# Performance work log

Hardware: AMD Instinct MI355X
Metric: run time of the kernel (lower is better)

The kernel has to match this reference:

```python
import jax, jax.numpy as jnp
import numpy as np

B, S, D, H, E, K, F = 2, 2048, 1024, 16, 8, 2, 4096
DH = D // H
EPS = 1e-5


def setup_inputs() -> dict:
    key = jax.random.key(0)
    ks = jax.random.split(key, 10)
    init = lambda k, shape, scale: (jax.random.normal(k, shape, jnp.float32) * scale)
    s_d = D ** -0.5
    s_f = F ** -0.5
    return {
        "x": init(ks[0], (B, S, D), 1.0),
        "attn_mask": jnp.tril(jnp.ones((S, S), bool)),  # causal boolean mask
        "wq": init(ks[1], (D, D), s_d),
        "wk": init(ks[2], (D, D), s_d),
        "wv": init(ks[3], (D, D), s_d),
        "wo": init(ks[4], (D, D), s_d),
        "ln1_g": jnp.ones((D,), jnp.float32),
        "ln1_b": jnp.zeros((D,), jnp.float32),
        "ln2_g": jnp.ones((D,), jnp.float32),
        "ln2_b": jnp.zeros((D,), jnp.float32),
        "gate_w": init(ks[5], (D, E), s_d),
        "e_w1": init(ks[6], (E, D, F), s_d),
        "e_b1": jnp.zeros((E, F), jnp.float32),
        "e_w2": init(ks[7], (E, F, D), s_f),
        "e_b2": jnp.zeros((E, D), jnp.float32),
    }


def _ln(x, g, b):
    m = x.mean(-1, keepdims=True)
    v = ((x - m) ** 2).mean(-1, keepdims=True)
    return (x - m) * jax.lax.rsqrt(v + EPS) * g + b


def _mha(x, attn_mask, wq, wk, wv, wo):
    # x: [B,S,D] -> q,k,v: [B,H,S,DH]
    q = (x @ wq).reshape(B, S, H, DH).transpose(0, 2, 1, 3)
    k = (x @ wk).reshape(B, S, H, DH).transpose(0, 2, 1, 3)
    v = (x @ wv).reshape(B, S, H, DH).transpose(0, 2, 1, 3)
    scores = jnp.einsum("bhqd,bhkd->bhqk", q, k) * (DH ** -0.5)
    scores = jnp.where(attn_mask, scores, jnp.finfo(scores.dtype).min)
    attn = jax.nn.softmax(scores, axis=-1)
    o = jnp.einsum("bhqk,bhkd->bhqd", attn, v)
    return o.transpose(0, 2, 1, 3).reshape(B, S, D) @ wo


def _moe(x, gate_w, e_w1, e_b1, e_w2, e_b2):
    tokens = x.reshape(-1, D)  # [N,D]
    logits = tokens @ gate_w   # [N,E]
    vals, idx = jax.lax.top_k(logits, K)
    tw = jax.nn.softmax(vals, axis=-1)  # softmax over selected top-k logits
    # dense per-token expert weight matrix [N,E] (zero for unselected experts)
    w_dense = (jax.nn.one_hot(idx, E, dtype=tokens.dtype) * tw[..., None]).sum(1)

    def step(acc, p):
        w1, b1, w2, b2, we = p
        h = jax.nn.gelu(tokens @ w1 + b1)
        return acc + (h @ w2 + b2) * we[:, None], None

    combined, _ = jax.lax.scan(
        step, jnp.zeros_like(tokens), (e_w1, e_b1, e_w2, e_b2, w_dense.T)
    )
    return combined.reshape(x.shape)


def reference(x, attn_mask, wq, wk, wv, wo, ln1_g, ln1_b, ln2_g, ln2_b,
              gate_w, e_w1, e_b1, e_w2, e_b2):
    x = _ln(x, ln1_g, ln1_b)
    x = x + _mha(x, attn_mask, wq, wk, wv, wo)  # dropout p=0.0
    x = _ln(x, ln2_g, ln2_b)
    x = x + _moe(x, gate_w, e_w1, e_b1, e_w2, e_b2)
    return x
```

## Files before the change

kernel.cpp:

```cpp
#include <hip/hip_runtime.h>
#include <math.h>
#include <stdint.h>

typedef __attribute__((ext_vector_type(8))) short short8;
typedef __attribute__((ext_vector_type(4))) float f32x4;
typedef __attribute__((ext_vector_type(4))) unsigned short u16x4;

#define NB 2
#define NS 2048
#define ND 1024
#define NH 16
#define NDH 64
#define NE 8
#define NF 4096
#define NTOK 4096
#define MAXBLK 72

__device__ __forceinline__ float bf2f(unsigned short u) {
  union { float f; uint32_t i; } x; x.i = ((uint32_t)u) << 16; return x.f;
}
__device__ __forceinline__ unsigned short f2bf(float f) {
  union { float f; uint32_t i; } x; x.f = f;
  uint32_t r = x.i + 0x7fffu + ((x.i >> 16) & 1u);
  return (unsigned short)(r >> 16);
}
struct bfp { unsigned short h, l; };
__device__ __forceinline__ bfp splitf(float x) {
  bfp r;
  r.h = f2bf(x);
  r.l = f2bf(x - bf2f(r.h));
  return r;
}
__device__ __forceinline__ float gelu_f(float x) {
  float u = 0.7978845608028654f * (x + 0.044715f * x * x * x);
  return 0.5f * x * (1.0f + tanhf(u));
}
#define MFMA(a, b, c) __builtin_amdgcn_mfma_f32_16x16x32_bf16(a, b, c, 0, 0, 0)
__device__ __forceinline__ f32x4 mfma4(short8 ah, short8 al, short8 bh, short8 bl,
                                       f32x4 c) {
  c = MFMA(ah, bh, c);
  c = MFMA(ah, bl, c);
  c = MFMA(al, bh, c);
  c = MFMA(al, bl, c);
  return c;
}

__device__ __forceinline__ void gld16(const unsigned short* g, unsigned short* l) {
  __builtin_amdgcn_global_load_lds(
      (__attribute__((address_space(1))) void*)(const void*)g,
      (__attribute__((address_space(3))) void*)l, 16, 0, 0);
}


__device__ __forceinline__ void setup_src4(
    const unsigned short* base_rows, size_t stride, int lane, int wid,
    const unsigned short* src[4]) {
#pragma unroll
  for (int j = 0; j < 4; j++) {
    int r = wid * 32 + j * 8 + (lane >> 3);
    src[j] = base_rows + (size_t)r * stride + (((lane & 7) ^ (r & 7)) << 3);
  }
}

__device__ __forceinline__ short8 ldsfrag(const unsigned short* lds, int row,
                                          int kk, int quad) {
  int byte = row * 128 + kk * 64 + quad * 16;
  byte ^= (row & 7) << 4;
  return *(const short8*)((const char*)lds + byte);
}

__device__ __forceinline__ void bsplit_mainloop(
    const unsigned short* ah_s[4], const unsigned short* al_s[4],
    const unsigned short* bh_s[4], const unsigned short* bl_s[4], int K,
    unsigned short* sAh, unsigned short* sAl,
    unsigned short* sBh, unsigned short* sBl, f32x4 acc[4][4]) {
  const int tid = threadIdx.x;
  const int lane = tid & 63, wid = tid >> 6;
  const int wy = wid >> 1, wx = wid & 1;
  const int col = lane & 15, quad = lane >> 4;
  unsigned short* dah = sAh + wid * 2048;
  unsigned short* dal = sAl + wid * 2048;
  unsigned short* dbh = sBh + wid * 2048;
  unsigned short* dbl = sBl + wid * 2048;
  for (int k0 = 0; k0 < K; k0 += 64) {
    __syncthreads();
#pragma unroll
    for (int j = 0; j < 4; j++) {
      gld16(ah_s[j] + k0, dah + j * 512);
      gld16(al_s[j] + k0, dal + j * 512);
      gld16(bh_s[j] + k0, dbh + j * 512);
      gld16(bl_s[j] + k0, dbl + j * 512);
    }
    __syncthreads();
#pragma unroll
    for (int kk = 0; kk < 2; kk++) {
      short8 ah[4], al[4], bh[4], bl[4];
#pragma unroll
      for (int mt = 0; mt < 4; mt++) {
        int row = wy * 64 + mt * 16 + col;
        ah[mt] = ldsfrag(sAh, row, kk, quad);
        al[mt] = ldsfrag(sAl, row, kk, quad);
      }
#pragma unroll
      for (int nt = 0; nt < 4; nt++) {
        int row = wx * 64 + nt * 16 + col;
        bh[nt] = ldsfrag(sBh, row, kk, quad);
        bl[nt] = ldsfrag(sBl, row, kk, quad);
      }
#pragma unroll
      for (int mt = 0; mt < 4; mt++)
#pragma unroll
        for (int nt = 0; nt < 4; nt++)
          acc[mt][nt] = mfma4(ah[mt], al[mt], bh[nt], bl[nt], acc[mt][nt]);
    }
  }
}

__device__ __forceinline__ void moe_mainloop(
    const unsigned short* a_s[4], const unsigned short* b_s[4], int K,
    unsigned short* As, unsigned short* Bs, f32x4 acc[4][4]) {
  const int tid = threadIdx.x;
  const int lane = tid & 63, wid = tid >> 6;
  const int wy = wid >> 1, wx = wid & 1;
  const int col = lane & 15, quad = lane >> 4;
  unsigned short* da = As + wid * 2048;
  unsigned short* db = Bs + wid * 2048;
  for (int k0 = 0; k0 < K; k0 += 64) {
    __syncthreads();
#pragma unroll
    for (int j = 0; j < 4; j++) {
      gld16(a_s[j] + k0, da + j * 512);
      gld16(b_s[j] + k0, db + j * 512);
    }
    __syncthreads();
#pragma unroll
    for (int kk = 0; kk < 2; kk++) {
      short8 af[4], bfv[4];
#pragma unroll
      for (int mt = 0; mt < 4; mt++)
        af[mt] = ldsfrag(As, wy * 64 + mt * 16 + col, kk, quad);
#pragma unroll
      for (int nt = 0; nt < 4; nt++)
        bfv[nt] = ldsfrag(Bs, wx * 64 + nt * 16 + col, kk, quad);
#pragma unroll
      for (int mt = 0; mt < 4; mt++)
#pragma unroll
        for (int nt = 0; nt < 4; nt++)
          acc[mt][nt] = MFMA(af[mt], bfv[nt], acc[mt][nt]);
    }
  }
}

__global__ __launch_bounds__(256) void ln_kernel(
    const float* __restrict__ x, const float* __restrict__ g,
    const float* __restrict__ b, unsigned short* __restrict__ out_h,
    unsigned short* __restrict__ out_l, unsigned short* __restrict__ out_b16,
    float* __restrict__ out_f) {
  int row = blockIdx.x;
  int tid = threadIdx.x;
  const float* xr = x + (size_t)row * ND;
  f32x4 v = *(const f32x4*)(xr + tid * 4);
  float s = v[0] + v[1] + v[2] + v[3];
  float s2 = v[0]*v[0] + v[1]*v[1] + v[2]*v[2] + v[3]*v[3];
  for (int o = 1; o < 64; o <<= 1) { s += __shfl_xor(s, o); s2 += __shfl_xor(s2, o); }
  __shared__ float red[8];
  if ((tid & 63) == 0) { red[tid >> 6] = s; red[4 + (tid >> 6)] = s2; }
  __syncthreads();
  s = red[0] + red[1] + red[2] + red[3];
  s2 = red[4] + red[5] + red[6] + red[7];
  float mean = s * (1.0f / ND);
  float var = s2 * (1.0f / ND) - mean * mean;
  float rstd = rsqrtf(var + 1e-5f);
  f32x4 gg = *(const f32x4*)(g + tid * 4);
  f32x4 bb = *(const f32x4*)(b + tid * 4);
  f32x4 of;
#pragma unroll
  for (int j = 0; j < 4; j++) of[j] = (v[j] - mean) * rstd * gg[j] + bb[j];
  *(f32x4*)(out_f + (size_t)row * ND + tid * 4) = of;
  if (out_h) {
    u16x4 oh, ol;
#pragma unroll
    for (int j = 0; j < 4; j++) { bfp t = splitf(of[j]); oh[j] = t.h; ol[j] = t.l; }
    *(u16x4*)(out_h + (size_t)row * ND + tid * 4) = oh;
    *(u16x4*)(out_l + (size_t)row * ND + tid * 4) = ol;
  }
  if (out_b16) {
    u16x4 ob;
#pragma unroll
    for (int j = 0; j < 4; j++) ob[j] = f2bf(of[j]);
    *(u16x4*)(out_b16 + (size_t)row * ND + tid * 4) = ob;
  }
}

__global__ __launch_bounds__(256) void transpose_wsplit(
    const float* __restrict__ in, unsigned short* __restrict__ outh,
    unsigned short* __restrict__ outl, int R, int C) {
  __shared__ float tile[64][68];
  int r0 = blockIdx.y * 64, c0 = blockIdx.x * 64;
  int lr = threadIdx.x >> 3, lc = (threadIdx.x & 7) * 8;
#pragma unroll
  for (int p = 0; p < 2; p++) {
    int r = lr + p * 32;
    const float* s = in + (size_t)(r0 + r) * C + c0 + lc;
    *(f32x4*)&tile[r][lc] = *(const f32x4*)s;
    *(f32x4*)&tile[r][lc + 4] = *(const f32x4*)(s + 4);
  }
  __syncthreads();
#pragma unroll
  for (int p = 0; p < 2; p++) {
    int c = lr + p * 32;
    u16x4 h0, h1, l0, l1;
#pragma unroll
    for (int i = 0; i < 4; i++) {
      bfp t0 = splitf(tile[lc + i][c]);
      bfp t1 = splitf(tile[lc + 4 + i][c]);
      h0[i] = t0.h; l0[i] = t0.l;
      h1[i] = t1.h; l1[i] = t1.l;
    }
    unsigned short* dh = outh + (size_t)(c0 + c) * R + r0 + lc;
    unsigned short* dl = outl + (size_t)(c0 + c) * R + r0 + lc;
    *(u16x4*)dh = h0; *(u16x4*)(dh + 4) = h1;
    *(u16x4*)dl = l0; *(u16x4*)(dl + 4) = l1;
  }
}

__global__ __launch_bounds__(256) void transpose_w(
    const float* __restrict__ in, unsigned short* __restrict__ out,
    int R, int C) {
  __shared__ unsigned short tile[64][72];
  const float* src = in + (size_t)blockIdx.z * R * C;
  unsigned short* dst = out + (size_t)blockIdx.z * R * C;
  int r0 = blockIdx.y * 64, c0 = blockIdx.x * 64;
  int lr = threadIdx.x >> 3, lc = (threadIdx.x & 7) * 8;
#pragma unroll
  for (int p = 0; p < 2; p++) {
    int r = lr + p * 32;
    const float* s = src + (size_t)(r0 + r) * C + c0 + lc;
    f32x4 a = *(const f32x4*)s;
    f32x4 b = *(const f32x4*)(s + 4);
    u16x4 t0, t1;
#pragma unroll
    for (int j = 0; j < 4; j++) { t0[j] = f2bf(a[j]); t1[j] = f2bf(b[j]); }
    *(u16x4*)&tile[r][lc] = t0;
    *(u16x4*)&tile[r][lc + 4] = t1;
  }
  __syncthreads();
#pragma unroll
  for (int p = 0; p < 2; p++) {
    int c = lr + p * 32;
    union { unsigned short s[8]; f32x4 v; } t;
#pragma unroll
    for (int i = 0; i < 8; i++) t.s[i] = tile[lc + i][c];
    *(f32x4*)(dst + (size_t)(c0 + c) * R + r0 + lc) = t.v;
  }
}

__global__ __launch_bounds__(256) void transpose_v_split(
    const float* __restrict__ v_lin, unsigned short* __restrict__ vth,
    unsigned short* __restrict__ vtl) {
  __shared__ float tile[64][68];
  int bh = blockIdx.y, b = bh >> 4, h = bh & 15;
  int s0 = blockIdx.x * 64;
  int lr = threadIdx.x >> 3, lc = (threadIdx.x & 7) * 8;
#pragma unroll
  for (int p = 0; p < 2; p++) {
    int s = lr + p * 32;
    const float* src = v_lin + (size_t)(b * NS + s0 + s) * ND + h * NDH + lc;
    *(f32x4*)&tile[s][lc] = *(const f32x4*)src;
    *(f32x4*)&tile[s][lc + 4] = *(const f32x4*)(src + 4);
  }
  __syncthreads();
#pragma unroll
  for (int p = 0; p < 2; p++) {
    int dh = lr + p * 32;
    u16x4 h0, h1, l0, l1;
#pragma unroll
    for (int i = 0; i < 4; i++) {
      bfp t0 = splitf(tile[lc + i][dh]);
      bfp t1 = splitf(tile[lc + 4 + i][dh]);
      h0[i] = t0.h; l0[i] = t0.l;
      h1[i] = t1.h; l1[i] = t1.l;
    }
    unsigned short* dh_p = vth + (size_t)(bh * NDH + dh) * NS + s0 + lc;
    unsigned short* dl_p = vtl + (size_t)(bh * NDH + dh) * NS + s0 + lc;
    *(u16x4*)dh_p = h0; *(u16x4*)(dh_p + 4) = h1;
    *(u16x4*)dl_p = l0; *(u16x4*)(dl_p + 4) = l1;
  }
}

__global__ __launch_bounds__(256, 2) void gemm_qkv(
    const unsigned short* __restrict__ Xh, const unsigned short* __restrict__ Xl,
    const unsigned short* __restrict__ wqh, const unsigned short* __restrict__ wql,
    const unsigned short* __restrict__ wkh, const unsigned short* __restrict__ wkl,
    const unsigned short* __restrict__ wvh, const unsigned short* __restrict__ wvl,
    unsigned short* __restrict__ qh, unsigned short* __restrict__ ql,
    unsigned short* __restrict__ kh, unsigned short* __restrict__ kl,
    float* __restrict__ vf) {
  __shared__ __attribute__((aligned(16))) unsigned short sAh[8192];
  __shared__ __attribute__((aligned(16))) unsigned short sAl[8192];
  __shared__ __attribute__((aligned(16))) unsigned short sBh[8192];
  __shared__ __attribute__((aligned(16))) unsigned short sBl[8192];
  int z = blockIdx.z;
  const unsigned short* Bh = (z == 0) ? wqh : (z == 1) ? wkh : wvh;
  const unsigned short* Bl = (z == 0) ? wql : (z == 1) ? wkl : wvl;
  unsigned short* oh = (z == 0) ? qh : kh;
  unsigned short* ol = (z == 0) ? ql : kl;
  int m0 = blockIdx.y * 128, n0 = blockIdx.x * 128;
  int tid = threadIdx.x;
  int lane = tid & 63, wid = tid >> 6;
  const unsigned short* ah_s[4];
  const unsigned short* al_s[4];
  const unsigned short* bh_s[4];
  const unsigned short* bl_s[4];
  setup_src4(Xh + (size_t)m0 * ND, ND, lane, wid, ah_s);
  setup_src4(Xl + (size_t)m0 * ND, ND, lane, wid, al_s);
  setup_src4(Bh + (size_t)n0 * ND, ND, lane, wid, bh_s);
  setup_src4(Bl + (size_t)n0 * ND, ND, lane, wid, bl_s);
  f32x4 acc[4][4];
#pragma unroll
  for (int mt = 0; mt < 4; mt++)
#pragma unroll
    for (int nt = 0; nt < 4; nt++) acc[mt][nt] = (f32x4){0.f, 0.f, 0.f, 0.f};
  bsplit_mainloop(ah_s, al_s, bh_s, bl_s, ND, sAh, sAl, sBh, sBl, acc);
  int wy = wid >> 1, wx = wid & 1;
  int col = lane & 15, quad = lane >> 4;
#pragma unroll
  for (int mt = 0; mt < 4; mt++)
#pragma unroll
    for (int nt = 0; nt < 4; nt++)
#pragma unroll
      for (int r = 0; r < 4; r++) {
        int gr = m0 + wy * 64 + mt * 16 + quad * 4 + r;
        int gc = n0 + wx * 64 + nt * 16 + col;
        float v = acc[mt][nt][r];
        if (z == 2) {
          vf[(size_t)gr * ND + gc] = v;
        } else {
          bfp t = splitf(v);
          oh[(size_t)gr * ND + gc] = t.h;
          ol[(size_t)gr * ND + gc] = t.l;
        }
      }
}

__global__ __launch_bounds__(256, 2) void gemm_oproj(
    const unsigned short* __restrict__ Ah, const unsigned short* __restrict__ Al,
    const unsigned short* __restrict__ Bh, const unsigned short* __restrict__ Bl,
    const float* __restrict__ res, float* __restrict__ Cf) {
  __shared__ __attribute__((aligned(16))) unsigned short sAh[8192];
  __shared__ __attribute__((aligned(16))) unsigned short sAl[8192];
  __shared__ __attribute__((aligned(16))) unsigned short sBh[8192];
  __shared__ __attribute__((aligned(16))) unsigned short sBl[8192];
  int m0 = blockIdx.y * 128, n0 = blockIdx.x * 128;
  int tid = threadIdx.x;
  int lane = tid & 63, wid = tid >> 6;
  const unsigned short* ah_s[4];
  const unsigned short* al_s[4];
  const unsigned short* bh_s[4];
  const unsigned short* bl_s[4];
  setup_src4(Ah + (size_t)m0 * ND, ND, lane, wid, ah_s);
  setup_src4(Al + (size_t)m0 * ND, ND, lane, wid, al_s);
  setup_src4(Bh + (size_t)n0 * ND, ND, lane, wid, bh_s);
  setup_src4(Bl + (size_t)n0 * ND, ND, lane, wid, bl_s);
  f32x4 acc[4][4];
#pragma unroll
  for (int mt = 0; mt < 4; mt++)
#pragma unroll
    for (int nt = 0; nt < 4; nt++) acc[mt][nt] = (f32x4){0.f, 0.f, 0.f, 0.f};
  bsplit_mainloop(ah_s, al_s, bh_s, bl_s, ND, sAh, sAl, sBh, sBl, acc);
  int wy = wid >> 1, wx = wid & 1;
  int col = lane & 15, quad = lane >> 4;
#pragma unroll
  for (int mt = 0; mt < 4; mt++)
#pragma unroll
    for (int nt = 0; nt < 4; nt++)
#pragma unroll
      for (int r = 0; r < 4; r++) {
        int gr = m0 + wy * 64 + mt * 16 + quad * 4 + r;
        int gc = n0 + wx * 64 + nt * 16 + col;
        Cf[(size_t)gr * ND + gc] = acc[mt][nt][r] + res[(size_t)gr * ND + gc];
      }
}

__global__ __launch_bounds__(256, 2) void attn_kernel(
    const unsigned short* __restrict__ qh_g, const unsigned short* __restrict__ ql_g,
    const unsigned short* __restrict__ kh_g, const unsigned short* __restrict__ kl_g,
    const unsigned short* __restrict__ vth_g, const unsigned short* __restrict__ vtl_g,
    unsigned short* __restrict__ oh_g, unsigned short* __restrict__ ol_g) {
  __shared__ unsigned short Kh[64 * 72];
  __shared__ unsigned short Kl[64 * 72];
  __shared__ unsigned short Vh[64 * 72];
  __shared__ unsigned short Vl[64 * 72];
  __shared__ unsigned short Ph[64 * 72];
  __shared__ unsigned short Pl[64 * 72];
  int bh = blockIdx.y, b = bh >> 4, h = bh & 15;
  int tid = threadIdx.x, lane = tid & 63, w = tid >> 6;
  int col = lane & 15, quad = lane >> 4;
  int lr = tid >> 3, lc = (tid & 7) * 8;

  const unsigned short* kbh = kh_g + (size_t)b * NS * ND + h * NDH + lc;
  const unsigned short* kbl = kl_g + (size_t)b * NS * ND + h * NDH + lc;
  const unsigned short* vbh = vth_g + (size_t)bh * NDH * NS;
  const unsigned short* vbl = vtl_g + (size_t)bh * NDH * NS;

#pragma unroll 1
  for (int pass = 0; pass < 2; pass++) {
    int qt = (pass == 0) ? (int)blockIdx.x : 31 - (int)blockIdx.x;
    int q0 = qt * 64;

    size_t qoff = (size_t)(b * NS + q0 + w * 16 + col) * ND + h * NDH;
    short8 qh0 = *(const short8*)(qh_g + qoff + quad * 8);
    short8 qh1 = *(const short8*)(qh_g + qoff + 32 + quad * 8);
    short8 ql0 = *(const short8*)(ql_g + qoff + quad * 8);
    short8 ql1 = *(const short8*)(ql_g + qoff + 32 + quad * 8);

    f32x4 Oa[4];
#pragma unroll
    for (int nt = 0; nt < 4; nt++) Oa[nt] = (f32x4){0.f, 0.f, 0.f, 0.f};
    float mrow[4] = {-1e30f, -1e30f, -1e30f, -1e30f};
    float lrow[4] = {0.f, 0.f, 0.f, 0.f};

    for (int j = 0; j <= qt; j++) {
      __syncthreads();
#pragma unroll
      for (int p = 0; p < 2; p++) {
        int r = lr + p * 32;
        size_t ko = (size_t)(j * 64 + r) * ND;
        size_t vo = (size_t)r * NS + j * 64 + lc;
        *(f32x4*)(Kh + r * 72 + lc) = *(const f32x4*)(kbh + ko);
        *(f32x4*)(Kl + r * 72 + lc) = *(const f32x4*)(kbl + ko);
        *(f32x4*)(Vh + r * 72 + lc) = *(const f32x4*)(vbh + vo);
        *(f32x4*)(Vl + r * 72 + lc) = *(const f32x4*)(vbl + vo);
      }
      __syncthreads();
      f32x4 sf[4];
      __builtin_amdgcn_s_setprio(1);
#pragma unroll
      for (int nt = 0; nt < 4; nt++) {
        int o0 = (nt * 16 + col) * 72 + quad * 8;
        f32x4 a = (f32x4){0.f, 0.f, 0.f, 0.f};
        a = mfma4(qh0, ql0, *(const short8*)(Kh + o0), *(const short8*)(Kl + o0), a);
        a = mfma4(qh1, ql1, *(const short8*)(Kh + o0 + 32), *(const short8*)(Kl + o0 + 32), a);
        sf[nt] = a;
      }
      __builtin_amdgcn_s_setprio(0);
      bool diag = (j == qt);
#pragma unroll
      for (int nt = 0; nt < 4; nt++)
#pragma unroll
        for (int r = 0; r < 4; r++) {
          float v = sf[nt][r] * 0.125f;
          if (diag) {
            int rq = w * 16 + quad * 4 + r;
            int ck = nt * 16 + col;
            if (ck > rq) v = -1e30f;
          }
          sf[nt][r] = v;
        }
#pragma unroll
      for (int r = 0; r < 4; r++) {
        float mx = fmaxf(fmaxf(sf[0][r], sf[1][r]), fmaxf(sf[2][r], sf[3][r]));
        mx = fmaxf(mx, __shfl_xor(mx, 1));
        mx = fmaxf(mx, __shfl_xor(mx, 2));
        mx = fmaxf(mx, __shfl_xor(mx, 4));
        mx = fmaxf(mx, __shfl_xor(mx, 8));
        float mn = fmaxf(mrow[r], mx);
        float al = __expf(mrow[r] - mn);
        mrow[r] = mn;
        float ps = 0.f;
#pragma unroll
        for (int nt = 0; nt < 4; nt++) {
          float p = __expf(sf[nt][r] - mn);
          sf[nt][r] = p;
          ps += p;
        }
        ps += __shfl_xor(ps, 1);
        ps += __shfl_xor(ps, 2);
        ps += __shfl_xor(ps, 4);
        ps += __shfl_xor(ps, 8);
        lrow[r] = lrow[r] * al + ps;
#pragma unroll
        for (int nt = 0; nt < 4; nt++) Oa[nt][r] *= al;
      }
#pragma unroll
      for (int nt = 0; nt < 4; nt++)
#pragma unroll
        for (int r = 0; r < 4; r++) {
          bfp t = splitf(sf[nt][r]);
          int o = (w * 16 + quad * 4 + r) * 72 + nt * 16 + col;
          Ph[o] = t.h;
          Pl[o] = t.l;
        }
      __syncthreads();
      int po = (w * 16 + col) * 72 + quad * 8;
      short8 pf0h = *(const short8*)(Ph + po);
      short8 pf0l = *(const short8*)(Pl + po);
      short8 pf1h = *(const short8*)(Ph + po + 32);
      short8 pf1l = *(const short8*)(Pl + po + 32);
      __builtin_amdgcn_s_setprio(1);
#pragma unroll
      for (int nt = 0; nt < 4; nt++) {
        int o0 = (nt * 16 + col) * 72 + quad * 8;
        Oa[nt] = mfma4(pf0h, pf0l, *(const short8*)(Vh + o0), *(const short8*)(Vl + o0), Oa[nt]);
        Oa[nt] = mfma4(pf1h, pf1l, *(const short8*)(Vh + o0 + 32), *(const short8*)(Vl + o0 + 32), Oa[nt]);
      }
      __builtin_amdgcn_s_setprio(0);
    }
#pragma unroll
    for (int nt = 0; nt < 4; nt++)
#pragma unroll
      for (int r = 0; r < 4; r++) {
        int gr = q0 + w * 16 + quad * 4 + r;
        int gc = nt * 16 + col;
        float ov = Oa[nt][r] / lrow[r];
        bfp t = splitf(ov);
        size_t oo = (size_t)(b * NS + gr) * ND + h * NDH + gc;
        oh_g[oo] = t.h;
        ol_g[oo] = t.l;
      }
  }
}

__global__ __launch_bounds__(256, 2) void gemm_moe1(
    const unsigned short* __restrict__ x3b, const unsigned short* __restrict__ w1t,
    const float* __restrict__ b1, const int* __restrict__ blk_e,
    const int* __restrict__ blk_mend, const int* __restrict__ tok_list,
    unsigned short* __restrict__ h) {
  __shared__ __attribute__((aligned(16))) unsigned short As[8192];
  __shared__ __attribute__((aligned(16))) unsigned short Bs[8192];
  int e = blk_e[blockIdx.y];
  if (e < 0) return;
  int mend = blk_mend[blockIdx.y];
  int m0 = blockIdx.y * 128, n0 = blockIdx.x * 128;
  int tid = threadIdx.x;
  int lane = tid & 63, wid = tid >> 6;
  const unsigned short* a_s[4];
  const unsigned short* b_s[4];
#pragma unroll
  for (int j = 0; j < 4; j++) {
    int r = wid * 32 + j * 8 + (lane >> 3);
    int gidx = m0 + r;
    int cl = gidx < (mend - 1) ? gidx : (mend - 1);
    int tok = tok_list[cl];
    a_s[j] = x3b + (size_t)tok * ND + (((lane & 7) ^ (r & 7)) << 3);
  }
  setup_src4(w1t + (size_t)e * NF * ND + (size_t)n0 * ND, ND, lane, wid, b_s);
  f32x4 acc[4][4];
#pragma unroll
  for (int mt = 0; mt < 4; mt++)
#pragma unroll
    for (int nt = 0; nt < 4; nt++) acc[mt][nt] = (f32x4){0.f, 0.f, 0.f, 0.f};
  moe_mainloop(a_s, b_s, ND, As, Bs, acc);
  int wy = wid >> 1, wx = wid & 1;
  int col = lane & 15, quad = lane >> 4;
#pragma unroll
  for (int mt = 0; mt < 4; mt++)
#pragma unroll
    for (int nt = 0; nt < 4; nt++)
#pragma unroll
      for (int r = 0; r < 4; r++) {
        int gr = m0 + wy * 64 + mt * 16 + quad * 4 + r;
        if (gr < mend) {
          int gc = n0 + wx * 64 + nt * 16 + col;
          float v = acc[mt][nt][r] + b1[e * NF + gc];
          h[(size_t)gr * NF + gc] = f2bf(gelu_f(v));
        }
      }
}

__global__ __launch_bounds__(256, 2) void gemm_moe2(
    const unsigned short* __restrict__ h, const unsigned short* __restrict__ w2t,
    const float* __restrict__ b2, const int* __restrict__ blk_e,
    const int* __restrict__ blk_mend, const int* __restrict__ tok_list,
    const float* __restrict__ w_list, float* __restrict__ out) {
  __shared__ __attribute__((aligned(16))) unsigned short As[8192];
  __shared__ __attribute__((aligned(16))) unsigned short Bs[8192];
  int e = blk_e[blockIdx.y];
  if (e < 0) return;
  int mend = blk_mend[blockIdx.y];
  int m0 = blockIdx.y * 128, n0 = blockIdx.x * 128;
  int tid = threadIdx.x;
  int lane = tid & 63, wid = tid >> 6;
  const unsigned short* a_s[4];
  const unsigned short* b_s[4];
  setup_src4(h + (size_t)m0 * NF, NF, lane, wid, a_s);
  setup_src4(w2t + (size_t)e * ND * NF + (size_t)n0 * NF, NF, lane, wid, b_s);
  f32x4 acc[4][4];
#pragma unroll
  for (int mt = 0; mt < 4; mt++)
#pragma unroll
    for (int nt = 0; nt < 4; nt++) acc[mt][nt] = (f32x4){0.f, 0.f, 0.f, 0.f};
  moe_mainloop(a_s, b_s, NF, As, Bs, acc);
  int wy = wid >> 1, wx = wid & 1;
  int col = lane & 15, quad = lane >> 4;
#pragma unroll
  for (int mt = 0; mt < 4; mt++)
#pragma unroll
    for (int nt = 0; nt < 4; nt++)
#pragma unroll
      for (int r = 0; r < 4; r++) {
        int gr = m0 + wy * 64 + mt * 16 + quad * 4 + r;
        if (gr < mend) {
          int gc = n0 + wx * 64 + nt * 16 + col;
          int tok = tok_list[gr];
          float wgt = w_list[gr];
          atomicAdd(&out[(size_t)tok * ND + gc],
                    wgt * (acc[mt][nt][r] + b2[e * ND + gc]));
        }
      }
}

__global__ __launch_bounds__(256) void gate_kernel(
    const float* __restrict__ x3f, const float* __restrict__ gw,
    int* __restrict__ e0a, int* __restrict__ e1a, float* __restrict__ w0a,
    float* __restrict__ w1a, int* __restrict__ cnt) {
  int t = (blockIdx.x * 256 + threadIdx.x) >> 6;
  int lane = threadIdx.x & 63;
  float acc[8] = {0, 0, 0, 0, 0, 0, 0, 0};
  const float* xr = x3f + (size_t)t * ND + lane * 16;
  f32x4 xv[4];
#pragma unroll
  for (int q = 0; q < 4; q++) xv[q] = *(const f32x4*)(xr + q * 4);
#pragma unroll
  for (int i = 0; i < 16; i++) {
    float xval = xv[i >> 2][i & 3];
    const float* grow = gw + (size_t)(lane * 16 + i) * NE;
    f32x4 g0 = *(const f32x4*)grow;
    f32x4 g1 = *(const f32x4*)(grow + 4);
#pragma unroll
    for (int e = 0; e < 4; e++) { acc[e] += xval * g0[e]; acc[4 + e] += xval * g1[e]; }
  }
#pragma unroll
  for (int e = 0; e < 8; e++)
    for (int o = 1; o < 64; o <<= 1) acc[e] += __shfl_xor(acc[e], o);
  if (lane == 0) {
    int i0 = 0;
    float m0 = acc[0];
#pragma unroll
    for (int e = 1; e < 8; e++)
      if (acc[e] > m0) { m0 = acc[e]; i0 = e; }
    int i1 = -1;
    float m1 = -1e30f;
#pragma unroll
    for (int e = 0; e < 8; e++)
      if (e != i0 && acc[e] > m1) { m1 = acc[e]; i1 = e; }
    float sw = __expf(m1 - m0);
    float w0 = 1.f / (1.f + sw);
    e0a[t] = i0; e1a[t] = i1; w0a[t] = w0; w1a[t] = 1.f - w0;
    atomicAdd(&cnt[i0], 1);
    atomicAdd(&cnt[i1], 1);
  }
}

__global__ void moe_scan(const int* __restrict__ cnt, int* __restrict__ seg_off,
                         int* __restrict__ blk_e, int* __restrict__ blk_mend) {
  if (threadIdx.x != 0 || blockIdx.x != 0) return;
  int o = 0, blk = 0;
  for (int e = 0; e < NE; e++) {
    seg_off[e] = o;
    int c = cnt[e];
    int nb = (c + 127) >> 7;
    for (int i = 0; i < nb; i++) { blk_e[blk] = e; blk_mend[blk] = o + c; blk++; }
    o += nb << 7;
  }
  for (; blk < MAXBLK; blk++) blk_e[blk] = -1;
}

__global__ __launch_bounds__(256) void gate_fill(
    const int* __restrict__ e0a, const int* __restrict__ e1a,
    const float* __restrict__ w0a, const float* __restrict__ w1a,
    const int* __restrict__ seg_off, int* __restrict__ fill,
    int* __restrict__ tok_list, float* __restrict__ w_list) {
  int t = blockIdx.x * 256 + threadIdx.x;
  if (t >= NTOK) return;
  int e0 = e0a[t];
  int p0 = seg_off[e0] + atomicAdd(&fill[e0], 1);
  tok_list[p0] = t;
  w_list[p0] = w0a[t];
  int e1 = e1a[t];
  int p1 = seg_off[e1] + atomicAdd(&fill[e1], 1);
  tok_list[p1] = t;
  w_list[p1] = w1a[t];
}

extern "C" void kernel_launch(void* const* d_in, const int* in_sizes, int n_in,
                              void* d_out, int out_size, void* d_ws, size_t ws_size,
                              hipStream_t stream) {
  const float* x = (const float*)d_in[0];
  const float* wq = (const float*)d_in[2];
  const float* wk = (const float*)d_in[3];
  const float* wv = (const float*)d_in[4];
  const float* wo = (const float*)d_in[5];
  const float* ln1g = (const float*)d_in[6];
  const float* ln1b = (const float*)d_in[7];
  const float* ln2g = (const float*)d_in[8];
  const float* ln2b = (const float*)d_in[9];
  const float* gatew = (const float*)d_in[10];
  const float* ew1 = (const float*)d_in[11];
  const float* eb1 = (const float*)d_in[12];
  const float* ew2 = (const float*)d_in[13];
  const float* eb2 = (const float*)d_in[14];
  float* out = (float*)d_out;
  uint8_t* ws = (uint8_t*)d_ws;

  constexpr size_t MB = 1048576;
  constexpr size_t X1F = 0;
  constexpr size_t X1H = 16 * MB;
  constexpr size_t X1L = 24 * MB;
  constexpr size_t QH = 32 * MB;
  constexpr size_t QL = 40 * MB;
  constexpr size_t KH = 48 * MB;
  constexpr size_t KL = 56 * MB;
  constexpr size_t VF = 64 * MB;
  constexpr size_t OH = 64 * MB;
  constexpr size_t OL = 72 * MB;
  constexpr size_t VTH = 80 * MB;
  constexpr size_t VTL = 88 * MB;
  constexpr size_t X2F = 96 * MB;
  constexpr size_t WQTH = 112 * MB;
  constexpr size_t WQTL = 114 * MB;
  constexpr size_t WKTH = 116 * MB;
  constexpr size_t WKTL = 118 * MB;
  constexpr size_t WVTH = 120 * MB;
  constexpr size_t WVTL = 122 * MB;
  constexpr size_t WOTH = 124 * MB;
  constexpr size_t WOTL = 126 * MB;
  constexpr size_t X3B = 128 * MB;
  constexpr size_t HBUF = 136 * MB;
  constexpr size_t W1T = 0;
  constexpr size_t W2T = 64 * MB;
  constexpr size_t CTRL = 208 * MB;
  constexpr size_t CNT = CTRL;
  constexpr size_t FILL = CNT + 32;
  constexpr size_t GE0 = CNT + 64;
  constexpr size_t GE1 = GE0 + 16384;
  constexpr size_t GW0 = GE1 + 16384;
  constexpr size_t GW1 = GW0 + 16384;
  constexpr size_t SEGO = GW1 + 16384;
  constexpr size_t BLKE = SEGO + 64;
  constexpr size_t BLKM = BLKE + 512;
  constexpr size_t TOKL = BLKM + 512;
  constexpr size_t WLST = TOKL + 36864;

  float* pX1F = (float*)(ws + X1F);
  unsigned short* pX1H = (unsigned short*)(ws + X1H);
  unsigned short* pX1L = (unsigned short*)(ws + X1L);
  unsigned short* pQH = (unsigned short*)(ws + QH);
  unsigned short* pQL = (unsigned short*)(ws + QL);
  unsigned short* pKH = (unsigned short*)(ws + KH);
  unsigned short* pKL = (unsigned short*)(ws + KL);
  float* pVF = (float*)(ws + VF);
  unsigned short* pOH = (unsigned short*)(ws + OH);
  unsigned short* pOL = (unsigned short*)(ws + OL);
  unsigned short* pVTH = (unsigned short*)(ws + VTH);
  unsigned short* pVTL = (unsigned short*)(ws + VTL);
  float* pX2F = (float*)(ws + X2F);
  unsigned short* pWQTH = (unsigned short*)(ws + WQTH);
  unsigned short* pWQTL = (unsigned short*)(ws + WQTL);
  unsigned short* pWKTH = (unsigned short*)(ws + WKTH);
  unsigned short* pWKTL = (unsigned short*)(ws + WKTL);
  unsigned short* pWVTH = (unsigned short*)(ws + WVTH);
  unsigned short* pWVTL = (unsigned short*)(ws + WVTL);
  unsigned short* pWOTH = (unsigned short*)(ws + WOTH);
  unsigned short* pWOTL = (unsigned short*)(ws + WOTL);
  unsigned short* pX3B = (unsigned short*)(ws + X3B);
  unsigned short* pH = (unsigned short*)(ws + HBUF);
  unsigned short* pW1T = (unsigned short*)(ws + W1T);
  unsigned short* pW2T = (unsigned short*)(ws + W2T);
  int* pCNT = (int*)(ws + CNT);
  int* pFILL = (int*)(ws + FILL);
  int* pGE0 = (int*)(ws + GE0);
  int* pGE1 = (int*)(ws + GE1);
  float* pGW0 = (float*)(ws + GW0);
  float* pGW1 = (float*)(ws + GW1);
  int* pSEGO = (int*)(ws + SEGO);
  int* pBLKE = (int*)(ws + BLKE);
  int* pBLKM = (int*)(ws + BLKM);
  int* pTOKL = (int*)(ws + TOKL);
  float* pWLST = (float*)(ws + WLST);

  (void)hipMemsetAsync(ws + CNT, 0, 64, stream);

  ln_kernel<<<NTOK, 256, 0, stream>>>(x, ln1g, ln1b, pX1H, pX1L, nullptr, pX1F);

  transpose_wsplit<<<dim3(16, 16), 256, 0, stream>>>(wq, pWQTH, pWQTL, 1024, 1024);
  transpose_wsplit<<<dim3(16, 16), 256, 0, stream>>>(wk, pWKTH, pWKTL, 1024, 1024);
  transpose_wsplit<<<dim3(16, 16), 256, 0, stream>>>(wv, pWVTH, pWVTL, 1024, 1024);
  transpose_wsplit<<<dim3(16, 16), 256, 0, stream>>>(wo, pWOTH, pWOTL, 1024, 1024);

  gemm_qkv<<<dim3(8, 32, 3), 256, 0, stream>>>(
      pX1H, pX1L, pWQTH, pWQTL, pWKTH, pWKTL, pWVTH, pWVTL,
      pQH, pQL, pKH, pKL, pVF);

  transpose_v_split<<<dim3(32, 32), 256, 0, stream>>>(pVF, pVTH, pVTL);
  attn_kernel<<<dim3(16, 32), 256, 0, stream>>>(pQH, pQL, pKH, pKL, pVTH, pVTL, pOH, pOL);
  gemm_oproj<<<dim3(8, 32), 256, 0, stream>>>(pOH, pOL, pWOTH, pWOTL, pX1F, pX2F);

  ln_kernel<<<NTOK, 256, 0, stream>>>(pX2F, ln2g, ln2b, nullptr, nullptr, pX3B, out);

  transpose_w<<<dim3(64, 16, 8), 256, 0, stream>>>(ew1, pW1T, 1024, 4096);
  transpose_w<<<dim3(16, 64, 8), 256, 0, stream>>>(ew2, pW2T, 4096, 1024);

  gate_kernel<<<1024, 256, 0, stream>>>(out, gatew, pGE0, pGE1, pGW0, pGW1, pCNT);
  moe_scan<<<1, 1, 0, stream>>>(pCNT, pSEGO, pBLKE, pBLKM);
  gate_fill<<<16, 256, 0, stream>>>(pGE0, pGE1, pGW0, pGW1, pSEGO, pFILL, pTOKL, pWLST);

  gemm_moe1<<<dim3(32, MAXBLK), 256, 0, stream>>>(pX3B, pW1T, eb1, pBLKE, pBLKM, pTOKL, pH);
  gemm_moe2<<<dim3(8, MAXBLK), 256, 0, stream>>>(pH, pW2T, eb2, pBLKE, pBLKM, pTOKL, pWLST, out);
}
```

Measured before the change: 1.024 ms.

## Double-buffer MoE GEMM LDS tiles and remap block IDs for XCD locality

The MoE expert GEMM main loop now uses two LDS buffer pairs, so global-to-LDS loads for the next K slice are issued before the MFMA work on the current slice. This aims to overlap memory latency with compute and removes one barrier per iteration. Separately, the QKV, out-projection and MoE GEMMs remap the linear block index so that blocks sent round-robin to the 8 XCDs work on contiguous row or column groups, which should improve L2 reuse. LDS use per MoE block doubles to 64 KB, which may reduce occupancy, and the remap assumes specific grid shapes (8 by 32, 32 by 72, 8 by 72).

```diff
diff --git a/kernel.cpp b/kernel.cpp
--- a/kernel.cpp
+++ b/kernel.cpp
@@ -116,38 +116,55 @@
   }
 }
 
-__device__ __forceinline__ void moe_mainloop(
-    const unsigned short* a_s[4], const unsigned short* b_s[4], int K,
-    unsigned short* As, unsigned short* Bs, f32x4 acc[4][4]) {
+__device__ __forceinline__ void moe_stage(
+    const unsigned short* const a_s[4], const unsigned short* const b_s[4],
+    int k0, unsigned short* As, unsigned short* Bs, int wid) {
+  unsigned short* da = As + wid * 2048;
+  unsigned short* db = Bs + wid * 2048;
+#pragma unroll
+  for (int j = 0; j < 4; j++) {
+    gld16(a_s[j] + k0, da + j * 512);
+    gld16(b_s[j] + k0, db + j * 512);
+  }
+}
+
+__device__ __forceinline__ void moe_compute(
+    const unsigned short* As, const unsigned short* Bs,
+    int wy, int wx, int col, int quad, f32x4 acc[4][4]) {
+#pragma unroll
+  for (int kk = 0; kk < 2; kk++) {
+    short8 af[4], bfv[4];
+#pragma unroll
+    for (int mt = 0; mt < 4; mt++)
+      af[mt] = ldsfrag(As, wy * 64 + mt * 16 + col, kk, quad);
+#pragma unroll
+    for (int nt = 0; nt < 4; nt++)
+      bfv[nt] = ldsfrag(Bs, wx * 64 + nt * 16 + col, kk, quad);
+#pragma unroll
+    for (int mt = 0; mt < 4; mt++)
+#pragma unroll
+      for (int nt = 0; nt < 4; nt++)
+        acc[mt][nt] = MFMA(af[mt], bfv[nt], acc[mt][nt]);
+  }
+}
+
+__device__ __forceinline__ void moe_mainloop_db(
+    const unsigned short* const a_s[4], const unsigned short* const b_s[4],
+    int K, unsigned short* As0, unsigned short* Bs0,
+    unsigned short* As1, unsigned short* Bs1, f32x4 acc[4][4]) {
   const int tid = threadIdx.x;
   const int lane = tid & 63, wid = tid >> 6;
   const int wy = wid >> 1, wx = wid & 1;
   const int col = lane & 15, quad = lane >> 4;
-  unsigned short* da = As + wid * 2048;
-  unsigned short* db = Bs + wid * 2048;
-  for (int k0 = 0; k0 < K; k0 += 64) {
+  moe_stage(a_s, b_s, 0, As0, Bs0, wid);
+  __syncthreads();
+  for (int k0 = 0; k0 < K; k0 += 128) {
+    moe_stage(a_s, b_s, k0 + 64, As1, Bs1, wid);
+    moe_compute(As0, Bs0, wy, wx, col, quad, acc);
     __syncthreads();
-#pragma unroll
-    for (int j = 0; j < 4; j++) {
-      gld16(a_s[j] + k0, da + j * 512);
-      gld16(b_s[j] + k0, db + j * 512);
-    }
+    if (k0 + 128 < K) moe_stage(a_s, b_s, k0 + 128, As0, Bs0, wid);
+    moe_compute(As1, Bs1, wy, wx, col, quad, acc);
     __syncthreads();
-#pragma unroll
-    for (int kk = 0; kk < 2; kk++) {
-      short8 af[4], bfv[4];
-#pragma unroll
-      for (int mt = 0; mt < 4; mt++)
-        af[mt] = ldsfrag(As, wy * 64 + mt * 16 + col, kk, quad);
-#pragma unroll
-      for (int nt = 0; nt < 4; nt++)
-        bfv[nt] = ldsfrag(Bs, wx * 64 + nt * 16 + col, kk, quad);
-#pragma unroll
-      for (int mt = 0; mt < 4; mt++)
-#pragma unroll
-        for (int nt = 0; nt < 4; nt++)
-          acc[mt][nt] = MFMA(af[mt], bfv[nt], acc[mt][nt]);
-    }
   }
 }
 
@@ -305,7 +322,11 @@
   const unsigned short* Bl = (z == 0) ? wql : (z == 1) ? wkl : wvl;
   unsigned short* oh = (z == 0) ? qh : kh;
   unsigned short* ol = (z == 0) ? ql : kl;
-  int m0 = blockIdx.y * 128, n0 = blockIdx.x * 128;
+  int kb = blockIdx.y * 8 + blockIdx.x;
+  int c = kb & 7, ii = kb >> 3;
+  int by = c * 4 + (ii >> 3);
+  int bx = ii & 7;
+  int m0 = by * 128, n0 = bx * 128;
   int tid = threadIdx.x;
   int lane = tid & 63, wid = tid >> 6;
   const unsigned short* ah_s[4];
@@ -351,7 +372,11 @@
   __shared__ __attribute__((aligned(16))) unsigned short sAl[8192];
   __shared__ __attribute__((aligned(16))) unsigned short sBh[8192];
   __shared__ __attribute__((aligned(16))) unsigned short sBl[8192];
-  int m0 = blockIdx.y * 128, n0 = blockIdx.x * 128;
+  int kb = blockIdx.y * 8 + blockIdx.x;
+  int c = kb & 7, ii = kb >> 3;
+  int by = c * 4 + (ii >> 3);
+  int bx = ii & 7;
+  int m0 = by * 128, n0 = bx * 128;
   int tid = threadIdx.x;
   int lane = tid & 63, wid = tid >> 6;
   const unsigned short* ah_s[4];
@@ -526,12 +551,18 @@
     const float* __restrict__ b1, const int* __restrict__ blk_e,
     const int* __restrict__ blk_mend, const int* __restrict__ tok_list,
     unsigned short* __restrict__ h) {
-  __shared__ __attribute__((aligned(16))) unsigned short As[8192];
-  __shared__ __attribute__((aligned(16))) unsigned short Bs[8192];
-  int e = blk_e[blockIdx.y];
+  __shared__ __attribute__((aligned(16))) unsigned short As0[8192];
+  __shared__ __attribute__((aligned(16))) unsigned short Bs0[8192];
+  __shared__ __attribute__((aligned(16))) unsigned short As1[8192];
+  __shared__ __attribute__((aligned(16))) unsigned short Bs1[8192];
+  int kb = blockIdx.y * 32 + blockIdx.x;
+  int c = kb & 7, ii = kb >> 3;
+  int bx = c * 4 + (ii / 72);
+  int by = ii % 72;
+  int e = blk_e[by];
   if (e < 0) return;
-  int mend = blk_mend[blockIdx.y];
-  int m0 = blockIdx.y * 128, n0 = blockIdx.x * 128;
+  int mend = blk_mend[by];
+  int m0 = by * 128, n0 = bx * 128;
   int tid = threadIdx.x;
   int lane = tid & 63, wid = tid >> 6;
   const unsigned short* a_s[4];
@@ -550,7 +581,7 @@
   for (int mt = 0; mt < 4; mt++)
 #pragma unroll
     for (int nt = 0; nt < 4; nt++) acc[mt][nt] = (f32x4){0.f, 0.f, 0.f, 0.f};
-  moe_mainloop(a_s, b_s, ND, As, Bs, acc);
+  moe_mainloop_db(a_s, b_s, ND, As0, Bs0, As1, Bs1, acc);
   int wy = wid >> 1, wx = wid & 1;
   int col = lane & 15, quad = lane >> 4;
 #pragma unroll
@@ -573,12 +604,18 @@
     const float* __restrict__ b2, const int* __restrict__ blk_e,
     const int* __restrict__ blk_mend, const int* __restrict__ tok_list,
     const float* __restrict__ w_list, float* __restrict__ out) {
-  __shared__ __attribute__((aligned(16))) unsigned short As[8192];
-  __shared__ __attribute__((aligned(16))) unsigned short Bs[8192];
-  int e = blk_e[blockIdx.y];
+  __shared__ __attribute__((aligned(16))) unsigned short As0[8192];
+  __shared__ __attribute__((aligned(16))) unsigned short Bs0[8192];
+  __shared__ __attribute__((aligned(16))) unsigned short As1[8192];
+  __shared__ __attribute__((aligned(16))) unsigned short Bs1[8192];
+  int kb = blockIdx.y * 8 + blockIdx.x;
+  int c = kb & 7, ii = kb >> 3;
+  int by = c * 9 + (ii >> 3);
+  int bx = ii & 7;
+  int e = blk_e[by];
   if (e < 0) return;
-  int mend = blk_mend[blockIdx.y];
-  int m0 = blockIdx.y * 128, n0 = blockIdx.x * 128;
+  int mend = blk_mend[by];
+  int m0 = by * 128, n0 = bx * 128;
   int tid = threadIdx.x;
   int lane = tid & 63, wid = tid >> 6;
   const unsigned short* a_s[4];
@@ -590,7 +627,7 @@
   for (int mt = 0; mt < 4; mt++)
 #pragma unroll
     for (int nt = 0; nt < 4; nt++) acc[mt][nt] = (f32x4){0.f, 0.f, 0.f, 0.f};
-  moe_mainloop(a_s, b_s, NF, As, Bs, acc);
+  moe_mainloop_db(a_s, b_s, NF, As0, Bs0, As1, Bs1, acc);
   int wy = wid >> 1, wx = wid & 1;
   int col = lane & 15, quad = lane >> 4;
 #pragma unroll
```

Result: slower. 1.075 ms (+5.0%).
